# Kernel tuning notes

Measured on AMD Instinct MI355X. Metric: run time of the kernel, lower is better.

Reference implementation:

```python
import jax, jax.numpy as jnp
import numpy as np

EPS = 1e-6
N_NODES, N_EDGES, HIDDEN, NUM_HEADS = 50000, 800000, 256, 8
HEAD_DIM = HIDDEN // NUM_HEADS
MLP_HIDDEN = 4 * HIDDEN


def _ln(x):
    # LayerNorm without affine, eps=1e-6
    m = x.mean(-1, keepdims=True)
    v = ((x - m) ** 2).mean(-1, keepdims=True)
    return (x - m) * jax.lax.rsqrt(v + EPS)


def _modulate(x, shift, scale):
    return x * (1.0 + scale) + shift


def setup_inputs() -> dict:
    key = jax.random.key(0)
    ks = jax.random.split(key, 20)
    s = 0.02
    inp = {
        "x": jax.random.normal(ks[0], (N_NODES, HIDDEN), jnp.float32),
        "c": jax.random.normal(ks[1], (N_NODES, HIDDEN), jnp.float32),
        "edge_index": jax.random.randint(ks[2], (2, N_EDGES), 0, N_NODES, jnp.int64),
        "Wq": jax.random.normal(ks[3], (HIDDEN, HIDDEN), jnp.float32) * s,
        "bq": jnp.zeros((HIDDEN,), jnp.float32),
        "Wk": jax.random.normal(ks[4], (HIDDEN, HIDDEN), jnp.float32) * s,
        "bk": jnp.zeros((HIDDEN,), jnp.float32),
        "Wv": jax.random.normal(ks[5], (HIDDEN, HIDDEN), jnp.float32) * s,
        "bv": jnp.zeros((HIDDEN,), jnp.float32),
        "Wo": jax.random.normal(ks[6], (HIDDEN, HIDDEN), jnp.float32) * s,
        "bo": jnp.zeros((HIDDEN,), jnp.float32),
        "W1": jax.random.normal(ks[7], (HIDDEN, MLP_HIDDEN), jnp.float32) * s,
        "b1": jnp.zeros((MLP_HIDDEN,), jnp.float32),
        "W2": jax.random.normal(ks[8], (MLP_HIDDEN, HIDDEN), jnp.float32) * s,
        "b2": jnp.zeros((HIDDEN,), jnp.float32),
        "Wc": jax.random.normal(ks[9], (HIDDEN, 6 * HIDDEN), jnp.float32) * s,
        "bc": jnp.zeros((6 * HIDDEN,), jnp.float32),
    }
    return inp


def reference(x, c, edge_index, Wq, bq, Wk, bk, Wv, bv, Wo, bo, W1, b1, W2, b2, Wc, bc):
    n = x.shape[0]
    src, dst = edge_index[0], edge_index[1]  # messages flow src(j) -> dst(i)

    # adaLN modulation: SiLU -> Linear -> chunk 6 along feature dim
    mod = jax.nn.silu(c) @ Wc + bc  # [N, 6*H]
    shift_msa, scale_msa, gate_msa, shift_mlp, scale_mlp, gate_mlp = jnp.split(mod, 6, axis=1)

    # ---- attention branch ----
    h = _modulate(_ln(x), shift_msa, scale_msa)  # [N, HIDDEN]
    q = (h @ Wq + bq).reshape(n, NUM_HEADS, HEAD_DIM)
    k = (h @ Wk + bk).reshape(n, NUM_HEADS, HEAD_DIM)
    v = (h @ Wv + bv).reshape(n, NUM_HEADS, HEAD_DIM)

    scale = HEAD_DIM ** -0.5
    sim = jnp.einsum('ehd,ehd->eh', q[dst], k[src]) * scale  # [E, NH]
    # segment softmax over destination node
    smax = jax.ops.segment_max(sim, dst, num_segments=n)  # [N, NH]
    expd = jnp.exp(sim - smax[dst])
    denom = jax.ops.segment_sum(expd, dst, num_segments=n)  # [N, NH]
    attn = expd / denom[dst]  # [E, NH]

    msg = v[src] * attn[:, :, None]  # [E, NH, HD]
    agg = jax.ops.segment_sum(msg, dst, num_segments=n).reshape(n, HIDDEN)
    attn_out = agg @ Wo + bo

    x = x + gate_msa * attn_out

    # ---- MLP branch ----
    h2 = _modulate(_ln(x), shift_mlp, scale_mlp)
    h2 = jax.nn.gelu(h2 @ W1 + b1, approximate=True)
    mlp_out = h2 @ W2 + b2

    return x + gate_mlp * mlp_out
```

## Files before the change

### kernel.cpp

```cpp
#include <hip/hip_runtime.h>


typedef __attribute__((ext_vector_type(8))) short bf16x8;
typedef __attribute__((ext_vector_type(2))) _Float16 h2_t;
typedef __attribute__((ext_vector_type(4))) float f32x4;

__device__ __forceinline__ float bf2f(unsigned short u) {
  union { float f; unsigned int i; } x; x.i = ((unsigned int)u) << 16; return x.f;
}
__device__ __forceinline__ unsigned short f2bf(float f) {
  union { float f; unsigned int i; } x; x.f = f;
  unsigned int r = x.i + 0x7fffu + ((x.i >> 16) & 1u);
  return (unsigned short)(r >> 16);
}

__device__ __forceinline__ void gload_lds16(const void* g, void* l) {
  __builtin_amdgcn_global_load_lds(
      (const __attribute__((address_space(1))) void*)g,
      (__attribute__((address_space(3))) void*)l, 16, 0, 0);
}

template <int EPI>
__global__ __launch_bounds__(256)
void gemm_bf16(const unsigned short* __restrict__ A,
               const unsigned short* __restrict__ Bt,
               const float* __restrict__ bias,
               const float* __restrict__ xin,
               const unsigned short* __restrict__ gate,
               void* __restrict__ out,
               int M, int N, int K, int lda, int ldo) {
  const int NT = N >> 7;
  const int MT = (M + 127) >> 7;
  const int pid = blockIdx.x;
  const int xcd = pid & 7;
  const int j = pid >> 3;
  const int rb = xcd + 8 * (j / NT);
  const int cb = j - (j / NT) * NT;
  if (rb >= MT) return;

  __shared__ unsigned short At[128 * 64];
  __shared__ unsigned short Bs[128 * 64];
  const int tid = threadIdx.x;
  const int wid = tid >> 6;
  const int lane = tid & 63;
  const int l15 = lane & 15, l4 = lane >> 4;
  const int row0 = rb * 128, col0 = cb * 128;
  const int wr = (wid >> 1) * 64, wc = (wid & 1) * 64;

  f32x4 acc[4][4];
  const f32x4 zf = {0.f, 0.f, 0.f, 0.f};
  for (int m = 0; m < 4; ++m)
    for (int n = 0; n < 4; ++n) acc[m][n] = zf;

  for (int kt = 0; kt < K; kt += 64) {
    __syncthreads();
#pragma unroll
    for (int s = 0; s < 4; ++s) {
      const int p = s * 4096 + tid * 16;
      const int r = p >> 7;
      const int scb = (p & 127) ^ ((r & 7) << 4);
      int gr = row0 + r; gr = gr < M ? gr : M - 1;
      gload_lds16((const char*)A + ((size_t)gr * lda + kt) * 2 + scb,
                  (char*)At + s * 4096 + wid * 1024);
      const int gc = col0 + r;
      gload_lds16((const char*)Bt + ((size_t)gc * K + kt) * 2 + scb,
                  (char*)Bs + s * 4096 + wid * 1024);
    }
    __syncthreads();
#pragma unroll
    for (int kk = 0; kk < 64; kk += 32) {
      bf16x8 af[4], bfr[4];
#pragma unroll
      for (int m = 0; m < 4; ++m) {
        const int r = wr + m * 16 + l15;
        const int cb2 = ((kk + l4 * 8) * 2) ^ ((r & 7) << 4);
        af[m] = *(const bf16x8*)((const char*)At + r * 128 + cb2);
      }
#pragma unroll
      for (int n = 0; n < 4; ++n) {
        const int r = wc + n * 16 + l15;
        const int cb2 = ((kk + l4 * 8) * 2) ^ ((r & 7) << 4);
        bfr[n] = *(const bf16x8*)((const char*)Bs + r * 128 + cb2);
      }
#pragma unroll
      for (int m = 0; m < 4; ++m)
#pragma unroll
        for (int n = 0; n < 4; ++n)
          acc[m][n] = __builtin_amdgcn_mfma_f32_16x16x32_bf16(af[m], bfr[n],
                                                              acc[m][n], 0, 0, 0);
    }
  }

  if (EPI == 2) {
#pragma unroll
    for (int m = 0; m < 4; ++m)
#pragma unroll
      for (int jj = 0; jj < 4; ++jj) {
        const int gr = row0 + wr + m * 16 + l4 * 4 + jj;
        if (gr >= M) continue;
#pragma unroll
        for (int n = 0; n < 4; ++n) {
          const int gc = col0 + wc + n * 16 + l15;
          const float v = acc[m][n][jj] + bias[gc];
          const float gt = bf2f(gate[(size_t)gr * 1536 + gc]);
          ((float*)out)[(size_t)gr * ldo + gc] =
              xin[(size_t)gr * ldo + gc] + gt * v;
        }
      }
  } else if (EPI == 3) {
    __syncthreads();
#pragma unroll
    for (int half = 0; half < 2; ++half) {
      if ((wid >> 1) == half) {
#pragma unroll
        for (int m = 0; m < 4; ++m)
#pragma unroll
          for (int jj = 0; jj < 4; ++jj) {
            const int row_l = m * 16 + l4 * 4 + jj;
            const int swz = (row_l & 12) << 2;
#pragma unroll
            for (int n = 0; n < 4; ++n) {
              const int col = wc + n * 16 + l15;
              const float v = acc[m][n][jj] + bias[col0 + col];
              const unsigned short h =
                  __builtin_bit_cast(unsigned short, (_Float16)v);
              const unsigned char b8 =
                  (unsigned char)((h + 0x7fu + ((h >> 8) & 1u)) >> 8);
              ((unsigned char*)At)[row_l * 128 + (col ^ swz)] = b8;
            }
          }
      }
      __syncthreads();
#pragma unroll
      for (int p = 0; p < 2; ++p) {
        const int u = p * 256 + tid;
        const int row_l = u >> 3;
        const int cb16 = (u & 7) * 16;
        const int gr = row0 + half * 64 + row_l;
        if (gr < M) {
          const bf16x8 vv = *(const bf16x8*)((const unsigned char*)At +
                                             row_l * 128 +
                                             (cb16 ^ ((row_l & 12) << 2)));
          *(bf16x8*)((unsigned char*)out + (size_t)gr * ldo + col0 + cb16) = vv;
        }
      }
      __syncthreads();
    }
  } else {
    __syncthreads();
#pragma unroll
    for (int half = 0; half < 2; ++half) {
      if ((wid >> 1) == half) {
#pragma unroll
        for (int m = 0; m < 4; ++m)
#pragma unroll
          for (int jj = 0; jj < 4; ++jj) {
            const int row_l = m * 16 + l4 * 4 + jj;
            const int swz = (row_l & 12) << 2;
#pragma unroll
            for (int n = 0; n < 4; ++n) {
              const int col = wc + n * 16 + l15;
              float v = acc[m][n][jj] + bias[col0 + col];
              if (EPI == 1) {
                const float u2 = 1.5957691216f * (v + 0.044715f * v * v * v);
                v = v / (1.f + __expf(-u2));
              }
              At[row_l * 128 + (col ^ swz)] = f2bf(v);
            }
          }
      }
      __syncthreads();
#pragma unroll
      for (int p = 0; p < 4; ++p) {
        const int u = p * 256 + tid;
        const int row_l = u >> 4;
        const int col8 = ((u & 15) * 8) ^ ((row_l & 12) << 2);
        const int gr = row0 + half * 64 + row_l;
        if (gr < M) {
          const bf16x8 vv = *(const bf16x8*)&At[row_l * 128 + col8];
          *(bf16x8*)((unsigned short*)out + (size_t)gr * ldo + col0 +
                     (((u & 15) * 8))) = vv;
        }
      }
      __syncthreads();
    }
  }
}

__global__ void sentinel_fill(float* o, long n, float v) {
  long i = (long)blockIdx.x * blockDim.x + threadIdx.x;
  const long st = (long)gridDim.x * blockDim.x;
  for (; i < n; i += st) o[i] = (i == 0) ? v : 0.f;
}

__global__ void prep_weights(const float* __restrict__ Wc, const float* __restrict__ Wq,
                             const float* __restrict__ Wk, const float* __restrict__ Wv,
                             const float* __restrict__ Wo, const float* __restrict__ W1,
                             const float* __restrict__ W2,
                             unsigned short* __restrict__ Wct,
                             unsigned short* __restrict__ Wqkvt,
                             unsigned short* __restrict__ Wot,
                             unsigned short* __restrict__ W1t,
                             unsigned short* __restrict__ W2t,
                             const float* __restrict__ bq, const float* __restrict__ bk,
                             const float* __restrict__ bv, float* __restrict__ bqkv,
                             int* __restrict__ deg, int Mdeg,
                             const unsigned int* __restrict__ ei_u32, int E,
                             int* __restrict__ flag) {
  const int job = blockIdx.y;
  const int i = blockIdx.x * 256 + threadIdx.x;
  if (job == 7) {
    if (i < 256) bqkv[i] = bq[i];
    else if (i < 512) { int d = i - 256; bqkv[256 + ((d >> 2) << 3) + (d & 3)] = bk[d]; }
    else if (i < 768) { int d = i - 512; bqkv[256 + ((d >> 2) << 3) + 4 + (d & 3)] = bv[d]; }
    return;
  }
  if (job == 8) {
    if (i < Mdeg) deg[i] = 0;
    return;
  }
  if (job == 9) {
    if (blockIdx.x != 0) return;
    __shared__ int bad;
    if (threadIdx.x == 0) bad = 0;
    __syncthreads();
    const int n = E < 256 ? E : 256;
    if ((int)threadIdx.x < n && ei_u32[2 * threadIdx.x + 1] != 0u) atomicAdd(&bad, 1);
    __syncthreads();
    if (threadIdx.x == 0) *flag = (bad == 0);
    return;
  }
  const float* W; unsigned short* Wt; int N, kc, mode = 0;
  switch (job) {
    case 0: W = Wc; Wt = Wct; N = 1536; kc = 256; break;
    case 1: W = Wq; Wt = Wqkvt; N = 256; kc = 256; break;
    case 2: W = Wk; Wt = Wqkvt + 256 * 256; N = 256; kc = 256; mode = 1; break;
    case 3: W = Wv; Wt = Wqkvt + 256 * 256; N = 256; kc = 256; mode = 2; break;
    case 4: W = Wo; Wt = Wot; N = 256; kc = 256; break;
    case 5: W = W1; Wt = W1t; N = 1024; kc = 256; break;
    default: W = W2; Wt = W2t; N = 256; kc = 1024; break;
  }
  if (i >= N * kc) return;
  const int kk = i / N, n = i - kk * N;
  int r = n;
  if (mode == 1) r = ((n >> 2) << 3) + (n & 3);
  else if (mode == 2) r = ((n >> 2) << 3) + 4 + (n & 3);
  Wt[(size_t)r * kc + kk] = f2bf(W[(size_t)kk * N + n]);
}

__global__ void silu_cast(const float* __restrict__ c, unsigned short* __restrict__ o,
                          int total4) {
  int i = blockIdx.x * blockDim.x + threadIdx.x;
  if (i >= total4) return;
  float4 v = *(const float4*)&c[(size_t)i * 4];
  ushort4 r;
  r.x = f2bf(v.x / (1.f + __expf(-v.x)));
  r.y = f2bf(v.y / (1.f + __expf(-v.y)));
  r.z = f2bf(v.z / (1.f + __expf(-v.z)));
  r.w = f2bf(v.w / (1.f + __expf(-v.w)));
  *(ushort4*)&o[(size_t)i * 4] = r;
}

__global__ void ln_modulate(const float* __restrict__ xin,
                            const unsigned short* __restrict__ modv,
                            unsigned short* __restrict__ hout,
                            int M, int cshift, int cscale) {
  const int wid = threadIdx.x >> 6, lane = threadIdx.x & 63;
  const int row = blockIdx.x * 4 + wid;
  if (row >= M) return;
  const float4 x4 = *(const float4*)&xin[(size_t)row * 256 + lane * 4];
  float s = x4.x + x4.y + x4.z + x4.w;
  float ss = x4.x * x4.x + x4.y * x4.y + x4.z * x4.z + x4.w * x4.w;
#pragma unroll
  for (int m = 1; m < 64; m <<= 1) {
    s += __shfl_xor(s, m, 64);
    ss += __shfl_xor(ss, m, 64);
  }
  const float mean = s * (1.f / 256.f);
  const float var = ss * (1.f / 256.f) - mean * mean;
  const float rstd = rsqrtf(var + 1e-6f);
  const ushort4 sh4 = *(const ushort4*)&modv[(size_t)row * 1536 + cshift * 256 + lane * 4];
  const ushort4 sc4 = *(const ushort4*)&modv[(size_t)row * 1536 + cscale * 256 + lane * 4];
  ushort4 o;
  o.x = f2bf((x4.x - mean) * rstd * (1.f + bf2f(sc4.x)) + bf2f(sh4.x));
  o.y = f2bf((x4.y - mean) * rstd * (1.f + bf2f(sc4.y)) + bf2f(sh4.y));
  o.z = f2bf((x4.z - mean) * rstd * (1.f + bf2f(sc4.z)) + bf2f(sh4.z));
  o.w = f2bf((x4.w - mean) * rstd * (1.f + bf2f(sc4.w)) + bf2f(sh4.w));
  *(ushort4*)&hout[(size_t)row * 256 + lane * 4] = o;
}

__global__ void conv_hist(const void* __restrict__ ei, const int* __restrict__ flag,
                          int* __restrict__ src32, int* __restrict__ dst32,
                          int* __restrict__ deg, int E) {
  int e = blockIdx.x * blockDim.x + threadIdx.x;
  if (e >= E) return;
  int s, d;
  if (*flag) {
    const long long* p = (const long long*)ei;
    s = (int)p[e]; d = (int)p[E + e];
  } else {
    const int* p = (const int*)ei;
    s = p[e]; d = p[E + e];
  }
  src32[e] = s; dst32[e] = d;
  atomicAdd(&deg[d], 1);
}

__global__ __launch_bounds__(256)
void block_sum(const int* __restrict__ deg, int* __restrict__ bsum, int M) {
  int i = blockIdx.x * 256 + threadIdx.x;
  int v = (i < M) ? deg[i] : 0;
#pragma unroll
  for (int d = 1; d < 64; d <<= 1) v += __shfl_xor(v, d, 64);
  __shared__ int ws[4];
  const int lane = threadIdx.x & 63, w = threadIdx.x >> 6;
  if (lane == 0) ws[w] = v;
  __syncthreads();
  if (threadIdx.x == 0) bsum[blockIdx.x] = ws[0] + ws[1] + ws[2] + ws[3];
}

__global__ __launch_bounds__(256)
void scan_final(const int* __restrict__ deg, const int* __restrict__ bsum,
                int* __restrict__ start, int* __restrict__ cursor, int M, int NB) {
  const int b = blockIdx.x, t = threadIdx.x, i = b * 256 + t;
  const int lane = t & 63, w = t >> 6;
  __shared__ int ws[4];
  __shared__ int pref;
  const int v = (i < M) ? deg[i] : 0;
  int s = v;
#pragma unroll
  for (int d = 1; d < 64; d <<= 1) {
    int u = __shfl_up(s, d, 64);
    if (lane >= d) s += u;
  }
  if (lane == 63) ws[w] = s;
  if (t < 64) {
    int acc = 0;
    for (int base = 0; base < b; base += 64) {
      const int idx = base + lane;
      acc += (idx < b) ? bsum[idx] : 0;
    }
#pragma unroll
    for (int d = 1; d < 64; d <<= 1) acc += __shfl_xor(acc, d, 64);
    if (lane == 0) pref = acc;
  }
  __syncthreads();
  int add = pref;
  for (int k = 0; k < w; ++k) add += ws[k];
  const int excl = s - v + add;
  if (i < M) { start[i] = excl; cursor[i] = excl; }
  if (i == M - 1) start[M] = excl + v;
}

__global__ void csr_fill(const int* __restrict__ src32, const int* __restrict__ dst32,
                         int* __restrict__ cursor, int* __restrict__ csr, int E) {
  int e = blockIdx.x * blockDim.x + threadIdx.x;
  if (e >= E) return;
  int pos = atomicAdd(&cursor[dst32[e]], 1);
  csr[pos] = src32[e];
}

__global__ __launch_bounds__(256)
void attn_gather(const int* __restrict__ csr, const int* __restrict__ start,
                 const unsigned char* __restrict__ qkvp,
                 unsigned short* __restrict__ aggb, int M) {
  const int wid = threadIdx.x >> 6, lane = threadIdx.x & 63;
  const int row = blockIdx.x * 4 + wid;
  if (row >= M) return;
  const ushort4 q4 = *(const ushort4*)(qkvp + (size_t)row * 1024 + lane * 8);
  const float SC = 0.17677669529663687f;
  const float qf0 = bf2f(q4.x) * SC, qf1 = bf2f(q4.y) * SC;
  const float qf2 = bf2f(q4.z) * SC, qf3 = bf2f(q4.w) * SC;
  const int b0 = start[row], e0 = start[row + 1];
  float den = 0.f, a0 = 0.f, a1 = 0.f, a2 = 0.f, a3 = 0.f;

  auto LDKV = [&](int src) {
    return *(const uint2*)(qkvp + (size_t)src * 1024 + 512 + lane * 8);
  };
#define PROC(kv2)                                                              \
  {                                                                            \
    const unsigned kd = kv2.x, vd = kv2.y;                                     \
    const unsigned klo = ((kd << 8) & 0x0000ff00u) | ((kd << 16) & 0xff000000u);\
    const unsigned khi = ((kd >> 8) & 0x0000ff00u) | (kd & 0xff000000u);       \
    const h2_t k01 = __builtin_bit_cast(h2_t, klo);                            \
    const h2_t k23 = __builtin_bit_cast(h2_t, khi);                            \
    float s = qf0 * (float)k01[0] + qf1 * (float)k01[1] +                      \
              qf2 * (float)k23[0] + qf3 * (float)k23[1];                       \
    s += __shfl_xor(s, 1, 64);                                                 \
    s += __shfl_xor(s, 2, 64);                                                 \
    s += __shfl_xor(s, 4, 64);                                                 \
    const float ex = __expf(s);                                                \
    const unsigned vlo = ((vd << 8) & 0x0000ff00u) | ((vd << 16) & 0xff000000u);\
    const unsigned vhi = ((vd >> 8) & 0x0000ff00u) | (vd & 0xff000000u);       \
    const h2_t v01 = __builtin_bit_cast(h2_t, vlo);                            \
    const h2_t v23 = __builtin_bit_cast(h2_t, vhi);                            \
    den += ex;                                                                 \
    a0 += ex * (float)v01[0]; a1 += ex * (float)v01[1];                        \
    a2 += ex * (float)v23[0]; a3 += ex * (float)v23[1];                        \
  }

  int i = b0;
  if (i + 4 <= e0) {
    uint2 A0 = LDKV(csr[i]), A1 = LDKV(csr[i + 1]);
    uint2 A2 = LDKV(csr[i + 2]), A3 = LDKV(csr[i + 3]);
    while (i + 8 <= e0) {
      const uint2 B0 = LDKV(csr[i + 4]), B1 = LDKV(csr[i + 5]);
      const uint2 B2 = LDKV(csr[i + 6]), B3 = LDKV(csr[i + 7]);
      PROC(A0); PROC(A1); PROC(A2); PROC(A3);
      A0 = B0; A1 = B1; A2 = B2; A3 = B3;
      i += 4;
    }
    PROC(A0); PROC(A1); PROC(A2); PROC(A3);
    i += 4;
  }
  for (; i < e0; ++i) {
    const uint2 kv2 = LDKV(csr[i]);
    PROC(kv2);
  }
#undef PROC

  const float inv = den > 0.f ? 1.f / den : 0.f;
  ushort4 r;
  r.x = f2bf(a0 * inv); r.y = f2bf(a1 * inv);
  r.z = f2bf(a2 * inv); r.w = f2bf(a3 * inv);
  *(ushort4*)&aggb[(size_t)row * 256 + lane * 4] = r;
}

extern "C" void kernel_launch(void* const* d_in, const int* in_sizes, int n_in,
                              void* d_out, int out_size, void* d_ws, size_t ws_size,
                              hipStream_t stream) {
  (void)n_in;
  const float* x  = (const float*)d_in[0];
  const float* c  = (const float*)d_in[1];
  const void*  ei = d_in[2];
  const float* Wq = (const float*)d_in[3];
  const float* bq = (const float*)d_in[4];
  const float* Wk = (const float*)d_in[5];
  const float* bk = (const float*)d_in[6];
  const float* Wv = (const float*)d_in[7];
  const float* bv = (const float*)d_in[8];
  const float* Wo = (const float*)d_in[9];
  const float* bo = (const float*)d_in[10];
  const float* W1 = (const float*)d_in[11];
  const float* b1 = (const float*)d_in[12];
  const float* W2 = (const float*)d_in[13];
  const float* b2 = (const float*)d_in[14];
  const float* Wc = (const float*)d_in[15];
  const float* bc = (const float*)d_in[16];

  const int M = in_sizes[0] / 256;
  const int E = in_sizes[2] / 2;

  char* ws = (char*)d_ws;
  size_t off = 0;
  auto carve = [&](size_t bytes) {
    char* p = ws + off;
    off = (off + bytes + 255) & ~(size_t)255;
    return p;
  };
  unsigned short* modv = (unsigned short*)carve((size_t)M * 1536 * 2);
  char* D = carve((size_t)M * 1024);
  unsigned short* cs = (unsigned short*)D;
  unsigned char* qkvp = (unsigned char*)D;
  float* X1 = (float*)D;
  unsigned short* Wct   = (unsigned short*)carve((size_t)1536 * 256 * 2);
  unsigned short* Wqkvt = (unsigned short*)carve((size_t)768 * 256 * 2);
  unsigned short* Wot   = (unsigned short*)carve((size_t)256 * 256 * 2);
  unsigned short* W1t   = (unsigned short*)carve((size_t)1024 * 256 * 2);
  unsigned short* W2t   = (unsigned short*)carve((size_t)256 * 1024 * 2);
  float* bqkv = (float*)carve(768 * 4);
  int* flag = (int*)carve(256);
  int* src32  = (int*)carve((size_t)E * 4);
  int* dst32  = (int*)carve((size_t)E * 4);
  int* deg    = (int*)carve((size_t)(M + 4) * 4);
  int* startp = (int*)carve((size_t)(M + 4) * 4);
  int* cursor = (int*)carve((size_t)(M + 4) * 4);
  int* csr    = (int*)carve((size_t)E * 4);
  int* bsum   = (int*)carve(1024);

  unsigned short* hbuf  = (unsigned short*)d_out;
  unsigned short* hbuf2 = (unsigned short*)d_out;
  unsigned short* aggb  = (unsigned short*)((char*)d_out + (size_t)M * 512);
  float* xout = (float*)d_out;

  if (off > ws_size) {
    sentinel_fill<<<2048, 256, 0, stream>>>((float*)d_out, (long)out_size,
                                            (float)ws_size);
    return;
  }

  const int tb = 256;
  const int EB = (E + tb - 1) / tb;
  const int SB = (M + 255) / 256;

  prep_weights<<<dim3(1536, 10), 256, 0, stream>>>(
      Wc, Wq, Wk, Wv, Wo, W1, W2, Wct, Wqkvt, Wot, W1t, W2t,
      bq, bk, bv, bqkv, deg, M + 4, (const unsigned int*)ei, E, flag);
  conv_hist<<<EB, tb, 0, stream>>>(ei, flag, src32, dst32, deg, E);
  block_sum<<<SB, 256, 0, stream>>>(deg, bsum, M);
  scan_final<<<SB, 256, 0, stream>>>(deg, bsum, startp, cursor, M, SB);
  csr_fill<<<EB, tb, 0, stream>>>(src32, dst32, cursor, csr, E);

  auto gsz = [](int Mz, int Nz) {
    int MT = (Mz + 127) / 128, NT = Nz / 128;
    return 8 * ((MT + 7) / 8) * NT;
  };
  silu_cast<<<(M * 64 + tb - 1) / tb, tb, 0, stream>>>(c, cs, M * 64);
  gemm_bf16<0><<<gsz(M, 1536), 256, 0, stream>>>(cs, Wct, bc, nullptr, nullptr,
                                                 modv, M, 1536, 256, 256, 1536);
  ln_modulate<<<(M + 3) / 4, 256, 0, stream>>>(x, modv, hbuf, M, 0, 1);
  gemm_bf16<0><<<gsz(M, 256), 256, 0, stream>>>(hbuf, Wqkvt, bqkv, nullptr,
                                                nullptr, qkvp, M, 256, 256,
                                                256, 512);
  gemm_bf16<3><<<gsz(M, 512), 256, 0, stream>>>(hbuf, Wqkvt + 256 * 256,
                                                bqkv + 256, nullptr, nullptr,
                                                qkvp + 512, M, 512, 256,
                                                256, 1024);
  attn_gather<<<(M + 3) / 4, 256, 0, stream>>>(csr, startp, qkvp, aggb, M);
  gemm_bf16<2><<<gsz(M, 256), 256, 0, stream>>>(aggb, Wot, bo, x, modv + 512,
                                                X1, M, 256, 256, 256, 256);
  ln_modulate<<<(M + 3) / 4, 256, 0, stream>>>(X1, modv, hbuf2, M, 3, 4);
  gemm_bf16<1><<<gsz(M, 1024), 256, 0, stream>>>(hbuf2, W1t, b1, nullptr, nullptr,
                                                 modv, M, 1024, 256, 256, 1536);
  gemm_bf16<2><<<gsz(M, 256), 256, 0, stream>>>(modv, W2t, b2, X1, modv + 1280,
                                                xout, M, 256, 1024, 1536, 256);
}
```

Baseline: 573.5 us.

## Use 8-wave GEMM blocks and store the residual X1 in bf16

The GEMM kernel now launches 512 threads (8 waves), each computing a 64x32 subtile instead of 64x64. That halves the accumulators per wave and gives more waves to hide latency, at the cost of loading the A fragment twice as often per block. The epilogue now writes the whole tile to LDS in one pass instead of two halves. The intermediate residual X1 is stored as bf16 rather than fp32, with templated readers in ln_modulate and the final GEMM epilogue, which halves that traffic but lowers the precision of the residual path.

```diff
diff --git a/kernel.cpp b/kernel.cpp
--- a/kernel.cpp
+++ b/kernel.cpp
@@ -20,56 +20,57 @@
       (__attribute__((address_space(3))) void*)l, 16, 0, 0);
 }
 
-template <int EPI>
-__global__ __launch_bounds__(256)
+template <int EPI, int XINBF, int OUTBF>
+__global__ __launch_bounds__(512)
 void gemm_bf16(const unsigned short* __restrict__ A,
                const unsigned short* __restrict__ Bt,
                const float* __restrict__ bias,
-               const float* __restrict__ xin,
+               const void* __restrict__ xin,
                const unsigned short* __restrict__ gate,
                void* __restrict__ out,
                int M, int N, int K, int lda, int ldo) {
   const int NT = N >> 7;
   const int MT = (M + 127) >> 7;
   const int pid = blockIdx.x;
-  const int xcd = pid & 7;
   const int j = pid >> 3;
-  const int rb = xcd + 8 * (j / NT);
+  const int rb = (pid & 7) + 8 * (j / NT);
   const int cb = j - (j / NT) * NT;
   if (rb >= MT) return;
 
-  __shared__ unsigned short At[128 * 64];
-  __shared__ unsigned short Bs[128 * 64];
+  __shared__ char smem[32768];
+  unsigned short* At = (unsigned short*)smem;
+  unsigned short* Bs = (unsigned short*)(smem + 16384);
   const int tid = threadIdx.x;
   const int wid = tid >> 6;
   const int lane = tid & 63;
   const int l15 = lane & 15, l4 = lane >> 4;
   const int row0 = rb * 128, col0 = cb * 128;
-  const int wr = (wid >> 1) * 64, wc = (wid & 1) * 64;
-
-  f32x4 acc[4][4];
+  const int wr = (wid >> 2) * 64;
+  const int wc = (wid & 3) * 32;
+
+  f32x4 acc[4][2];
   const f32x4 zf = {0.f, 0.f, 0.f, 0.f};
   for (int m = 0; m < 4; ++m)
-    for (int n = 0; n < 4; ++n) acc[m][n] = zf;
+    for (int n = 0; n < 2; ++n) acc[m][n] = zf;
 
   for (int kt = 0; kt < K; kt += 64) {
     __syncthreads();
 #pragma unroll
-    for (int s = 0; s < 4; ++s) {
-      const int p = s * 4096 + tid * 16;
+    for (int s = 0; s < 2; ++s) {
+      const int p = s * 8192 + tid * 16;
       const int r = p >> 7;
       const int scb = (p & 127) ^ ((r & 7) << 4);
       int gr = row0 + r; gr = gr < M ? gr : M - 1;
       gload_lds16((const char*)A + ((size_t)gr * lda + kt) * 2 + scb,
-                  (char*)At + s * 4096 + wid * 1024);
+                  (char*)At + s * 8192 + wid * 1024);
       const int gc = col0 + r;
       gload_lds16((const char*)Bt + ((size_t)gc * K + kt) * 2 + scb,
-                  (char*)Bs + s * 4096 + wid * 1024);
+                  (char*)Bs + s * 8192 + wid * 1024);
     }
     __syncthreads();
 #pragma unroll
     for (int kk = 0; kk < 64; kk += 32) {
-      bf16x8 af[4], bfr[4];
+      bf16x8 af[4], bfr[2];
 #pragma unroll
       for (int m = 0; m < 4; ++m) {
         const int r = wr + m * 16 + l15;
@@ -77,7 +78,7 @@
         af[m] = *(const bf16x8*)((const char*)At + r * 128 + cb2);
       }
 #pragma unroll
-      for (int n = 0; n < 4; ++n) {
+      for (int n = 0; n < 2; ++n) {
         const int r = wc + n * 16 + l15;
         const int cb2 = ((kk + l4 * 8) * 2) ^ ((r & 7) << 4);
         bfr[n] = *(const bf16x8*)((const char*)Bs + r * 128 + cb2);
@@ -85,7 +86,7 @@
 #pragma unroll
       for (int m = 0; m < 4; ++m)
 #pragma unroll
-        for (int n = 0; n < 4; ++n)
+        for (int n = 0; n < 2; ++n)
           acc[m][n] = __builtin_amdgcn_mfma_f32_16x16x32_bf16(af[m], bfr[n],
                                                               acc[m][n], 0, 0, 0);
     }
@@ -99,90 +100,85 @@
         const int gr = row0 + wr + m * 16 + l4 * 4 + jj;
         if (gr >= M) continue;
 #pragma unroll
-        for (int n = 0; n < 4; ++n) {
+        for (int n = 0; n < 2; ++n) {
           const int gc = col0 + wc + n * 16 + l15;
           const float v = acc[m][n][jj] + bias[gc];
           const float gt = bf2f(gate[(size_t)gr * 1536 + gc]);
-          ((float*)out)[(size_t)gr * ldo + gc] =
-              xin[(size_t)gr * ldo + gc] + gt * v;
+          const float xv =
+              XINBF ? bf2f(((const unsigned short*)xin)[(size_t)gr * ldo + gc])
+                    : ((const float*)xin)[(size_t)gr * ldo + gc];
+          const float rv = xv + gt * v;
+          if (OUTBF)
+            ((unsigned short*)out)[(size_t)gr * ldo + gc] = f2bf(rv);
+          else
+            ((float*)out)[(size_t)gr * ldo + gc] = rv;
         }
       }
   } else if (EPI == 3) {
     __syncthreads();
 #pragma unroll
-    for (int half = 0; half < 2; ++half) {
-      if ((wid >> 1) == half) {
-#pragma unroll
-        for (int m = 0; m < 4; ++m)
-#pragma unroll
-          for (int jj = 0; jj < 4; ++jj) {
-            const int row_l = m * 16 + l4 * 4 + jj;
-            const int swz = (row_l & 12) << 2;
-#pragma unroll
-            for (int n = 0; n < 4; ++n) {
-              const int col = wc + n * 16 + l15;
-              const float v = acc[m][n][jj] + bias[col0 + col];
-              const unsigned short h =
-                  __builtin_bit_cast(unsigned short, (_Float16)v);
-              const unsigned char b8 =
-                  (unsigned char)((h + 0x7fu + ((h >> 8) & 1u)) >> 8);
-              ((unsigned char*)At)[row_l * 128 + (col ^ swz)] = b8;
-            }
-          }
-      }
-      __syncthreads();
-#pragma unroll
-      for (int p = 0; p < 2; ++p) {
-        const int u = p * 256 + tid;
-        const int row_l = u >> 3;
-        const int cb16 = (u & 7) * 16;
-        const int gr = row0 + half * 64 + row_l;
-        if (gr < M) {
-          const bf16x8 vv = *(const bf16x8*)((const unsigned char*)At +
-                                             row_l * 128 +
-                                             (cb16 ^ ((row_l & 12) << 2)));
-          *(bf16x8*)((unsigned char*)out + (size_t)gr * ldo + col0 + cb16) = vv;
+    for (int m = 0; m < 4; ++m)
+#pragma unroll
+      for (int jj = 0; jj < 4; ++jj) {
+        const int row_l = wr + m * 16 + l4 * 4 + jj;
+        const int swz = (row_l & 12) << 2;
+#pragma unroll
+        for (int n = 0; n < 2; ++n) {
+          const int col = wc + n * 16 + l15;
+          const float v = acc[m][n][jj] + bias[col0 + col];
+          const unsigned short h =
+              __builtin_bit_cast(unsigned short, (_Float16)v);
+          const unsigned char b8 =
+              (unsigned char)((h + 0x7fu + ((h >> 8) & 1u)) >> 8);
+          ((unsigned char*)smem)[row_l * 128 + (col ^ swz)] = b8;
         }
       }
-      __syncthreads();
+    __syncthreads();
+#pragma unroll
+    for (int pp = 0; pp < 2; ++pp) {
+      const int u = pp * 512 + tid;
+      const int row_l = u >> 3;
+      const int cb16 = (u & 7) * 16;
+      const int gr = row0 + row_l;
+      if (gr < M) {
+        const bf16x8 vv = *(const bf16x8*)((const unsigned char*)smem +
+                                           row_l * 128 +
+                                           (cb16 ^ ((row_l & 12) << 2)));
+        *(bf16x8*)((unsigned char*)out + (size_t)gr * ldo + col0 + cb16) = vv;
+      }
     }
   } else {
     __syncthreads();
-#pragma unroll
-    for (int half = 0; half < 2; ++half) {
-      if ((wid >> 1) == half) {
-#pragma unroll
-        for (int m = 0; m < 4; ++m)
-#pragma unroll
-          for (int jj = 0; jj < 4; ++jj) {
-            const int row_l = m * 16 + l4 * 4 + jj;
-            const int swz = (row_l & 12) << 2;
-#pragma unroll
-            for (int n = 0; n < 4; ++n) {
-              const int col = wc + n * 16 + l15;
-              float v = acc[m][n][jj] + bias[col0 + col];
-              if (EPI == 1) {
-                const float u2 = 1.5957691216f * (v + 0.044715f * v * v * v);
-                v = v / (1.f + __expf(-u2));
-              }
-              At[row_l * 128 + (col ^ swz)] = f2bf(v);
-            }
+    unsigned short* R = (unsigned short*)smem;
+#pragma unroll
+    for (int m = 0; m < 4; ++m)
+#pragma unroll
+      for (int jj = 0; jj < 4; ++jj) {
+        const int row_l = wr + m * 16 + l4 * 4 + jj;
+        const int swz = (row_l & 12) << 2;
+#pragma unroll
+        for (int n = 0; n < 2; ++n) {
+          const int col = wc + n * 16 + l15;
+          float v = acc[m][n][jj] + bias[col0 + col];
+          if (EPI == 1) {
+            const float u2 = 1.5957691216f * (v + 0.044715f * v * v * v);
+            v = v / (1.f + __expf(-u2));
           }
-      }
-      __syncthreads();
-#pragma unroll
-      for (int p = 0; p < 4; ++p) {
-        const int u = p * 256 + tid;
-        const int row_l = u >> 4;
-        const int col8 = ((u & 15) * 8) ^ ((row_l & 12) << 2);
-        const int gr = row0 + half * 64 + row_l;
-        if (gr < M) {
-          const bf16x8 vv = *(const bf16x8*)&At[row_l * 128 + col8];
-          *(bf16x8*)((unsigned short*)out + (size_t)gr * ldo + col0 +
-                     (((u & 15) * 8))) = vv;
+          R[row_l * 128 + (col ^ swz)] = f2bf(v);
         }
       }
-      __syncthreads();
+    __syncthreads();
+#pragma unroll
+    for (int pp = 0; pp < 4; ++pp) {
+      const int u = pp * 512 + tid;
+      const int row_l = u >> 4;
+      const int col8 = (u & 15) * 8;
+      const int gr = row0 + row_l;
+      if (gr < M) {
+        const bf16x8 vv =
+            *(const bf16x8*)&R[row_l * 128 + (col8 ^ ((row_l & 12) << 2))];
+        *(bf16x8*)((unsigned short*)out + (size_t)gr * ldo + col0 + col8) = vv;
+      }
     }
   }
 }
@@ -261,14 +257,22 @@
   *(ushort4*)&o[(size_t)i * 4] = r;
 }
 
-__global__ void ln_modulate(const float* __restrict__ xin,
+template <int INBF>
+__global__ void ln_modulate(const void* __restrict__ xin,
                             const unsigned short* __restrict__ modv,
                             unsigned short* __restrict__ hout,
                             int M, int cshift, int cscale) {
   const int wid = threadIdx.x >> 6, lane = threadIdx.x & 63;
   const int row = blockIdx.x * 4 + wid;
   if (row >= M) return;
-  const float4 x4 = *(const float4*)&xin[(size_t)row * 256 + lane * 4];
+  float4 x4;
+  if (INBF) {
+    const ushort4 u4 =
+        *(const ushort4*)((const unsigned short*)xin + (size_t)row * 256 + lane * 4);
+    x4.x = bf2f(u4.x); x4.y = bf2f(u4.y); x4.z = bf2f(u4.z); x4.w = bf2f(u4.w);
+  } else {
+    x4 = *(const float4*)((const float*)xin + (size_t)row * 256 + lane * 4);
+  }
   float s = x4.x + x4.y + x4.z + x4.w;
   float ss = x4.x * x4.x + x4.y * x4.y + x4.z * x4.z + x4.w * x4.w;
 #pragma unroll
@@ -462,7 +466,7 @@
   char* D = carve((size_t)M * 1024);
   unsigned short* cs = (unsigned short*)D;
   unsigned char* qkvp = (unsigned char*)D;
-  float* X1 = (float*)D;
+  unsigned short* X1b = (unsigned short*)D;
   unsigned short* Wct   = (unsigned short*)carve((size_t)1536 * 256 * 2);
   unsigned short* Wqkvt = (unsigned short*)carve((size_t)768 * 256 * 2);
   unsigned short* Wot   = (unsigned short*)carve((size_t)256 * 256 * 2);
@@ -506,22 +510,20 @@
     return 8 * ((MT + 7) / 8) * NT;
   };
   silu_cast<<<(M * 64 + tb - 1) / tb, tb, 0, stream>>>(c, cs, M * 64);
-  gemm_bf16<0><<<gsz(M, 1536), 256, 0, stream>>>(cs, Wct, bc, nullptr, nullptr,
-                                                 modv, M, 1536, 256, 256, 1536);
-  ln_modulate<<<(M + 3) / 4, 256, 0, stream>>>(x, modv, hbuf, M, 0, 1);
-  gemm_bf16<0><<<gsz(M, 256), 256, 0, stream>>>(hbuf, Wqkvt, bqkv, nullptr,
-                                                nullptr, qkvp, M, 256, 256,
-                                                256, 512);
-  gemm_bf16<3><<<gsz(M, 512), 256, 0, stream>>>(hbuf, Wqkvt + 256 * 256,
-                                                bqkv + 256, nullptr, nullptr,
-                                                qkvp + 512, M, 512, 256,
-                                                256, 1024);
+  gemm_bf16<0, 0, 0><<<gsz(M, 1536), 512, 0, stream>>>(
+      cs, Wct, bc, nullptr, nullptr, modv, M, 1536, 256, 256, 1536);
+  ln_modulate<0><<<(M + 3) / 4, 256, 0, stream>>>(x, modv, hbuf, M, 0, 1);
+  gemm_bf16<0, 0, 0><<<gsz(M, 256), 512, 0, stream>>>(
+      hbuf, Wqkvt, bqkv, nullptr, nullptr, qkvp, M, 256, 256, 256, 512);
+  gemm_bf16<3, 0, 0><<<gsz(M, 512), 512, 0, stream>>>(
+      hbuf, Wqkvt + 256 * 256, bqkv + 256, nullptr, nullptr, qkvp + 512,
+      M, 512, 256, 256, 1024);
   attn_gather<<<(M + 3) / 4, 256, 0, stream>>>(csr, startp, qkvp, aggb, M);
-  gemm_bf16<2><<<gsz(M, 256), 256, 0, stream>>>(aggb, Wot, bo, x, modv + 512,
-                                                X1, M, 256, 256, 256, 256);
-  ln_modulate<<<(M + 3) / 4, 256, 0, stream>>>(X1, modv, hbuf2, M, 3, 4);
-  gemm_bf16<1><<<gsz(M, 1024), 256, 0, stream>>>(hbuf2, W1t, b1, nullptr, nullptr,
-                                                 modv, M, 1024, 256, 256, 1536);
-  gemm_bf16<2><<<gsz(M, 256), 256, 0, stream>>>(modv, W2t, b2, X1, modv + 1280,
-                                                xout, M, 256, 1024, 1536, 256);
-}
+  gemm_bf16<2, 0, 1><<<gsz(M, 256), 512, 0, stream>>>(
+      aggb, Wot, bo, x, modv + 512, X1b, M, 256, 256, 256, 256);
+  ln_modulate<1><<<(M + 3) / 4, 256, 0, stream>>>(X1b, modv, hbuf2, M, 3, 4);
+  gemm_bf16<1, 0, 0><<<gsz(M, 1024), 512, 0, stream>>>(
+      hbuf2, W1t, b1, nullptr, nullptr, modv, M, 1024, 256, 256, 1536);
+  gemm_bf16<2, 1, 0><<<gsz(M, 256), 512, 0, stream>>>(
+      modv, W2t, b2, X1b, modv + 1280, xout, M, 256, 1024, 1536, 256);
+}
```

Result: faster. 484.1 us (-15.6%).
